# Performance work log

Measured on AMD Instinct MI355X. Metric: run time of the kernel, lower is better.

Reference implementation:

```python
import jax, jax.numpy as jnp
import numpy as np

# Model config (matches init_kwargs)
DATA_L = 256
LATENT_L = 64
LATENT_N = 8
N_COMPS = 8
LOG_2PI = float(np.log(2.0 * np.pi))


def setup_inputs() -> dict:
    key = jax.random.key(0)
    ks = jax.random.split(key, 7)
    B = 2048
    N = B * LATENT_N  # 16384
    x = jax.random.normal(ks[0], (B, DATA_L), dtype=jnp.float32)
    W_e = jax.random.normal(ks[1], (DATA_L, LATENT_L * N_COMPS * 3), dtype=jnp.float32) * 0.05
    b_e = jnp.zeros((LATENT_L * N_COMPS * 3,), dtype=jnp.float32)
    W_d = jax.random.normal(ks[2], (LATENT_L, DATA_L * N_COMPS * 3), dtype=jnp.float32) * 0.05
    b_d = jnp.zeros((DATA_L * N_COMPS * 3,), dtype=jnp.float32)
    u_e = jax.random.normal(ks[3], (N, LATENT_L), dtype=jnp.float32)
    r = jax.random.uniform(ks[4], (N, LATENT_L), dtype=jnp.float32)
    return {"x": x, "W_e": W_e, "b_e": b_e, "W_d": W_d, "b_d": b_d, "u_e": u_e, "r": r}


def _split3(pred, K, D):
    # pred: (N, 3*K*D) -> m, logp, loga each (N, K, D)
    m = pred[:, : K * D].reshape(-1, K, D)
    logp = pred[:, K * D : 2 * K * D].reshape(-1, K, D)
    loga = pred[:, 2 * K * D :].reshape(-1, K, D)
    loga = jax.nn.log_softmax(loga, axis=1)  # loga - logsumexp over comps
    return m, logp, loga


def _discrete_sample(loga, r):
    # loga: (N, K, D), r: (N, D). Matches torch: idx = sum((r > cumsum(p)).int(), dim=1)
    c = jnp.cumsum(jnp.exp(loga), axis=1)  # (N, K, D)
    idx = jnp.sum((r[:, None, :] > c).astype(jnp.int32), axis=1)  # (N, D)
    return jnp.clip(idx, 0, loga.shape[1] - 1)


def reference(x, W_e, b_e, W_d, b_d, u_e, r):
    K, L, D = N_COMPS, LATENT_L, DATA_L
    x_rep = jnp.tile(x, (LATENT_N, 1))  # (N, D)

    # Encoder (KAN with width=[data_l, 3*K*L] modeled as dense layer)
    pred_e = x_rep @ W_e + b_e  # (N, 3*K*L)
    m_e, logp_e, loga_e = _split3(pred_e, K, L)

    # Sample mixture component per (row, latent dim), gather, reparameterize
    idx = _discrete_sample(loga_e, r)  # (N, L) int32
    m_sel = jnp.take_along_axis(m_e, idx[:, None, :], axis=1)[:, 0, :]  # (N, L)
    logp_sel = jnp.take_along_axis(logp_e, idx[:, None, :], axis=1)[:, 0, :]
    h = m_sel + jnp.exp(-0.5 * logp_sel) * u_e  # (N, L)

    # log q(h|x): mixture-of-Gaussians density at h
    uh = jnp.exp(0.5 * logp_e) * (h[:, None, :] - m_e)  # (N, K, L)
    L_e = jax.nn.logsumexp(loga_e - 0.5 * uh * uh + 0.5 * logp_e, axis=1)  # (N, L)
    L_e = -0.5 * L * LOG_2PI + jnp.sum(L_e, axis=1)  # (N,)

    # log prior N(0, I)
    L_q = -0.5 * L * LOG_2PI - 0.5 * jnp.sum(h * h, axis=1)  # (N,)

    # Decoder mixture likelihood of x
    pred_d = h @ W_d + b_d  # (N, 3*K*D)
    m_d, logp_d, loga_d = _split3(pred_d, K, D)
    ux = jnp.exp(0.5 * logp_d) * (x_rep[:, None, :] - m_d)  # (N, K, D)
    L_d = jax.nn.logsumexp(loga_d - 0.5 * ux * ux + 0.5 * logp_d, axis=1)  # (N, D)
    L_d = -0.5 * D * LOG_2PI + jnp.sum(L_d, axis=1)  # (N,)

    return -jnp.mean(L_d + L_q - L_e)
```

## Files before the change

### kernel.cpp

```cpp
#include <hip/hip_runtime.h>
#include <hip/hip_bf16.h>
#include <math.h>

#define D_L   256
#define L_L   64
#define K_C   8
#define BATCH 2048
#define NTOT  16384
#define ENC_COLS 1536
#define DEC_COLS 6144
#define LOG2PI 1.8378770664093453f

typedef __attribute__((ext_vector_type(8)))  short  short8;
typedef __attribute__((ext_vector_type(8)))  unsigned short ushort8;
typedef __attribute__((ext_vector_type(4)))  float  float4_;
typedef __attribute__((ext_vector_type(16))) float  float16_;

#define OFF_PE   0
#define OFF_H    (BATCH * ENC_COLS)
#define OFF_LQE  (OFF_H + NTOT * L_L / 2)
#define OFF_LD   (OFF_LQE + NTOT)
#define OFF_XB   (OFF_LD + NTOT)
#define OFF_WET  (OFF_XB + BATCH * D_L / 2)
#define OFF_WDT  OFF_XB

__device__ __forceinline__ unsigned short f2bf(float f) {
  unsigned u = __float_as_uint(f);
  unsigned r = (u + 0x7fffu + ((u >> 16) & 1u)) >> 16;
  return (unsigned short)r;
}

__global__ __launch_bounds__(256) void k_cvt_x(
    const float* __restrict__ in, unsigned short* __restrict__ out)
{
  const size_t idx = ((size_t)blockIdx.x * 256 + threadIdx.x) * 8;
  float4_ a = *(const float4_*)(in + idx);
  float4_ b = *(const float4_*)(in + idx + 4);
  ushort8 o;
  o[0] = f2bf(a[0]); o[1] = f2bf(a[1]); o[2] = f2bf(a[2]); o[3] = f2bf(a[3]);
  o[4] = f2bf(b[0]); o[5] = f2bf(b[1]); o[6] = f2bf(b[2]); o[7] = f2bf(b[3]);
  *(ushort8*)(out + idx) = o;
}

__global__ __launch_bounds__(256) void k_cvt_T(
    const float* __restrict__ in, unsigned short* __restrict__ out,
    int R, int C)
{
  __shared__ float tile[64][65];
  const int t = threadIdx.x;
  const int c0 = blockIdx.x * 64, r0 = blockIdx.y * 64;
  {
    const int tr = t >> 2, tc = (t & 3) * 16;
    const float* src = in + (size_t)(r0 + tr) * C + c0 + tc;
    #pragma unroll
    for (int i = 0; i < 4; ++i) {
      float4_ v = *(const float4_*)(src + 4 * i);
      #pragma unroll
      for (int j = 0; j < 4; ++j) tile[tr][tc + 4 * i + j] = v[j];
    }
  }
  __syncthreads();
  const int c = t >> 2, ks = (t & 3) * 16;
  unsigned short tmp[16];
  #pragma unroll
  for (int j = 0; j < 16; ++j) tmp[j] = f2bf(tile[ks + j][c]);
  unsigned short* dst = out + (size_t)(c0 + c) * R + r0 + ks;
  ushort8 o0, o1;
  #pragma unroll
  for (int j = 0; j < 8; ++j) { o0[j] = tmp[j]; o1[j] = tmp[8 + j]; }
  *(ushort8*)dst = o0;
  *(ushort8*)(dst + 8) = o1;
}

__global__ __launch_bounds__(256) void k_enc_mfma(
    const unsigned short* __restrict__ xb, const unsigned short* __restrict__ WeT,
    const float* __restrict__ be, float* __restrict__ pe)
{
  __shared__ __align__(16) unsigned short as[64 * 264];
  __shared__ __align__(16) unsigned short bs[64 * 264];
  const int t = threadIdx.x;
  const int w = t >> 6, l = t & 63;
  const int m0 = blockIdx.y * 64, c0 = blockIdx.x * 64;

  #pragma unroll
  for (int p = 0; p < 8; ++p) {
    const int ci = t + 256 * p;
    const int row = ci >> 5, off = (ci & 31) * 8;
    *(ushort8*)&as[row * 264 + off] = *(const ushort8*)(xb + (size_t)(m0 + row) * 256 + off);
    *(ushort8*)&bs[row * 264 + off] = *(const ushort8*)(WeT + (size_t)(c0 + row) * 256 + off);
  }
  __syncthreads();

  const int lr = l & 15, lq = l >> 4;
  float4_ acc[4] = {};
  const unsigned short* aponce = &as[(w * 16 + lr) * 264 + lq * 8];
  #pragma unroll
  for (int kk = 0; kk < 8; ++kk) {
    short8 a = *(const short8*)(aponce + kk * 32);
    #pragma unroll
    for (int ct = 0; ct < 4; ++ct) {
      short8 b = *(const short8*)(&bs[(ct * 16 + lr) * 264 + lq * 8 + kk * 32]);
      acc[ct] = __builtin_amdgcn_mfma_f32_16x16x32_bf16(a, b, acc[ct], 0, 0, 0);
    }
  }
  #pragma unroll
  for (int ct = 0; ct < 4; ++ct) {
    const int c = c0 + ct * 16 + lr;
    const float bias = be[c];
    #pragma unroll
    for (int reg = 0; reg < 4; ++reg) {
      const int m = m0 + w * 16 + lq * 4 + reg;
      pe[(size_t)m * ENC_COLS + c] = acc[ct][reg] + bias;
    }
  }
}

__global__ __launch_bounds__(256) void k_enc_post(
    const float* __restrict__ pe, const float* __restrict__ ue,
    const float* __restrict__ rr, unsigned short* __restrict__ h,
    float* __restrict__ lqe)
{
  const int lane = threadIdx.x & 63;
  const int b = blockIdx.x * 4 + (threadIdx.x >> 6);
  const float* row = pe + (size_t)b * ENC_COLS + lane;

  float m[8], p[8], a[8];
  #pragma unroll
  for (int k = 0; k < K_C; ++k) {
    m[k] = row[k * 64]; p[k] = row[512 + k * 64]; a[k] = row[1024 + k * 64];
  }
  float amax = a[0];
  #pragma unroll
  for (int k = 1; k < K_C; ++k) amax = fmaxf(amax, a[k]);
  float sa = 0.f;
  #pragma unroll
  for (int k = 0; k < K_C; ++k) sa += __expf(a[k] - amax);
  const float lse_a = amax + __logf(sa);

  float cum[8];
  {
    float cs = 0.f;
    #pragma unroll
    for (int k = 0; k < K_C; ++k) { cs += __expf(a[k] - lse_a); cum[k] = cs; }
  }
  float ep[8];
  #pragma unroll
  for (int k = 0; k < K_C; ++k) ep[k] = __expf(p[k]);

  for (int j = 0; j < 8; ++j) {
    const int n = b + BATCH * j;
    const float rv = rr[(size_t)n * L_L + lane];
    const float uv = ue[(size_t)n * L_L + lane];
    int idx = 0;
    #pragma unroll
    for (int k = 0; k < K_C; ++k) idx += (rv > cum[k]) ? 1 : 0;
    idx = min(idx, K_C - 1);
    float msel = m[0], psel = p[0];
    #pragma unroll
    for (int k = 1; k < K_C; ++k) {
      const bool sel = (idx == k);
      msel = sel ? m[k] : msel;
      psel = sel ? p[k] : psel;
    }
    const float hv = fmaf(__expf(-0.5f * psel), uv, msel);
    h[(size_t)n * L_L + lane] = f2bf(hv);

    float st = 0.f;
    #pragma unroll
    for (int k = 0; k < K_C; ++k) {
      const float dd = hv - m[k];
      const float tt = a[k] + 0.5f * p[k] - 0.5f * ep[k] * dd * dd;
      st += __expf(tt);
    }
    float contrib = -0.5f * hv * hv - (__logf(st + 1e-30f) - lse_a);
    #pragma unroll
    for (int off = 32; off; off >>= 1) contrib += __shfl_xor(contrib, off, 64);
    if (lane == 0) lqe[n] = contrib;
  }
}

__global__ void k_zero(float* __restrict__ Ld)
{
  Ld[blockIdx.x * 256 + threadIdx.x] = 0.f;
}

__global__ __launch_bounds__(256) void k_dec_mfma(
    const unsigned short* __restrict__ hb, const float* __restrict__ x,
    const unsigned short* __restrict__ WdT, const float* __restrict__ bd,
    float* __restrict__ Ld)
{
  __shared__ __align__(16) unsigned short hs[64 * 72];
  __shared__ __align__(16) unsigned short bT[192 * 72];
  __shared__ float biasLds[192];

  const int t = threadIdx.x;
  const int w = t >> 6, l = t & 63;
  const int n0 = blockIdx.y * 64, d0 = blockIdx.x * 64;
  const int col = l & 31;
  const int q = l >> 5;
  const int rg = w >> 1;
  const int dg = w & 1;

  #pragma unroll
  for (int p = 0; p < 2; ++p) {
    const int ci = t + 256 * p;
    const int row = ci >> 3, off = (ci & 7) * 8;
    *(ushort8*)&hs[row * 72 + off] = *(const ushort8*)(hb + (size_t)(n0 + row) * 64 + off);
  }

  float xv[16];
  #pragma unroll
  for (int e = 0; e < 16; ++e) {
    const int rr_ = (e & 3) + 8 * (e >> 2) + 4 * q;
    const int n = n0 + rg * 32 + rr_;
    xv[e] = x[(size_t)(n & (BATCH - 1)) * D_L + d0 + dg * 32 + col];
  }

  float s_a[16], s_t[16];
  #pragma unroll
  for (int e = 0; e < 16; ++e) { s_a[e] = 0.f; s_t[e] = 0.f; }

  const unsigned short* arow = &hs[(rg * 32 + col) * 72 + q * 8];
  const unsigned short* brow = &bT[(dg * 32 + col) * 72 + q * 8];

  for (int kc = 0; kc < K_C; ++kc) {
    __syncthreads();
    #pragma unroll
    for (int p = 0; p < 6; ++p) {
      const int ci = t + 256 * p;
      const int c = ci >> 3, off = (ci & 7) * 8;
      const int param = c >> 6, dd = c & 63;
      *(ushort8*)&bT[c * 72 + off] =
          *(const ushort8*)(WdT + ((size_t)param * 2048 + kc * 256 + d0 + dd) * 64 + off);
    }
    if (t < 192) biasLds[t] = bd[(t >> 6) * 2048 + kc * 256 + d0 + (t & 63)];
    __syncthreads();

    float16_ am = {}, ap = {}, aa = {};
    #pragma unroll
    for (int st = 0; st < 4; ++st) {
      short8 af  = *(const short8*)(arow + st * 16);
      short8 bfm = *(const short8*)(brow + st * 16);
      short8 bfp = *(const short8*)(brow + 64 * 72 + st * 16);
      short8 bfa = *(const short8*)(brow + 128 * 72 + st * 16);
      am = __builtin_amdgcn_mfma_f32_32x32x16_bf16(af, bfm, am, 0, 0, 0);
      ap = __builtin_amdgcn_mfma_f32_32x32x16_bf16(af, bfp, ap, 0, 0, 0);
      aa = __builtin_amdgcn_mfma_f32_32x32x16_bf16(af, bfa, aa, 0, 0, 0);
    }

    const float bm_ = biasLds[dg * 32 + col];
    const float bp_ = biasLds[64 + dg * 32 + col];
    const float ba_ = biasLds[128 + dg * 32 + col];
    #pragma unroll
    for (int e = 0; e < 16; ++e) {
      const float lm = am[e] + bm_;
      const float lp = ap[e] + bp_;
      const float la = aa[e] + ba_;
      const float dd = xv[e] - lm;
      const float ex = __expf(lp);
      const float tt = fmaf(0.5f, lp, la) - 0.5f * ex * dd * dd;
      s_a[e] += __expf(la);
      s_t[e] += __expf(tt);
    }
  }

  #pragma unroll
  for (int e = 0; e < 16; ++e) {
    float v = __logf(s_t[e] + 1e-30f) - __logf(s_a[e]);
    v += __shfl_xor(v, 1, 64);
    v += __shfl_xor(v, 2, 64);
    v += __shfl_xor(v, 4, 64);
    v += __shfl_xor(v, 8, 64);
    v += __shfl_xor(v, 16, 64);
    if (col == 0) {
      const int rr_ = (e & 3) + 8 * (e >> 2) + 4 * q;
      atomicAdd(&Ld[n0 + rg * 32 + rr_], v);
    }
  }
}

__global__ __launch_bounds__(1024) void k_final(
    const float* __restrict__ Ld, const float* __restrict__ lqe,
    float* __restrict__ out)
{
  const int tid = threadIdx.x;
  float s = 0.f;
  for (int n = tid; n < NTOT; n += 1024) s += Ld[n] + lqe[n];
  #pragma unroll
  for (int off = 32; off; off >>= 1) s += __shfl_xor(s, off, 64);
  __shared__ float red[16];
  if ((tid & 63) == 0) red[tid >> 6] = s;
  __syncthreads();
  if (tid < 64) {
    float v = (tid < 16) ? red[tid] : 0.f;
    #pragma unroll
    for (int off = 8; off; off >>= 1) v += __shfl_xor(v, off, 64);
    if (tid == 0) out[0] = -(v / (float)NTOT) + 128.0f * LOG2PI;
  }
}

extern "C" void kernel_launch(void* const* d_in, const int* in_sizes, int n_in,
                              void* d_out, int out_size, void* d_ws, size_t ws_size,
                              hipStream_t stream)
{
  const float* x  = (const float*)d_in[0];
  const float* We = (const float*)d_in[1];
  const float* be = (const float*)d_in[2];
  const float* Wd = (const float*)d_in[3];
  const float* bd = (const float*)d_in[4];
  const float* ue = (const float*)d_in[5];
  const float* rr = (const float*)d_in[6];
  float* out = (float*)d_out;

  float* ws = (float*)d_ws;
  float* pe            = ws + OFF_PE;
  unsigned short* h    = (unsigned short*)(ws + OFF_H);
  float* lqe           = ws + OFF_LQE;
  float* Ld            = ws + OFF_LD;
  unsigned short* xb   = (unsigned short*)(ws + OFF_XB);
  unsigned short* WeT  = (unsigned short*)(ws + OFF_WET);
  unsigned short* WdT  = (unsigned short*)(ws + OFF_WDT);

  k_cvt_x<<<dim3(256), 256, 0, stream>>>(x, xb);
  k_cvt_T<<<dim3(ENC_COLS / 64, D_L / 64), 256, 0, stream>>>(We, WeT, D_L, ENC_COLS);
  k_zero<<<dim3(NTOT / 256), 256, 0, stream>>>(Ld);
  k_enc_mfma<<<dim3(ENC_COLS / 64, BATCH / 64), 256, 0, stream>>>(xb, WeT, be, pe);
  k_cvt_T<<<dim3(DEC_COLS / 64, 1), 256, 0, stream>>>(Wd, WdT, L_L, DEC_COLS);
  k_enc_post<<<dim3(BATCH / 4), 256, 0, stream>>>(pe, ue, rr, h, lqe);
  k_dec_mfma<<<dim3(4, NTOT / 64), 256, 0, stream>>>(h, x, WdT, bd, Ld);
  k_final<<<dim3(1), 1024, 0, stream>>>(Ld, lqe, out);
}
```

Before: 140.3 us.

## Restructure pipeline: merged prep kernel, async LDS loads, double-buffered decoder, scalar reduction

Replaces the eight-launch pipeline with five kernels. Weight conversions and accumulator zeroing move into one prep kernel, and the x-to-bf16 conversion is fused into the encoder GEMM, which now uses 32x32 MFMA with K-chunked staging. The decoder now handles 128 rows per block, loads tiles with global_load_lds into double-buffered XOR-swizzled LDS, folds bias and a log2e scale into weights for exp2/log2 math, and reduces straight to one scalar with atomics. This removes launches, intermediate arrays and per-row atomics, at the cost of higher register and LDS use and a non-deterministic float atomic sum.

```diff
diff --git a/kernel.cpp b/kernel.cpp
--- a/kernel.cpp
+++ b/kernel.cpp
@@ -8,120 +8,160 @@
 #define BATCH 2048
 #define NTOT  16384
 #define ENC_COLS 1536
-#define DEC_COLS 6144
 #define LOG2PI 1.8378770664093453f
-
-typedef __attribute__((ext_vector_type(8)))  short  short8;
+#define L2E    1.4426950408889634f
+#define LN2    0.6931471805599453f
+#define C_HL2E 0.7213475204444817f
+
+typedef __attribute__((ext_vector_type(8)))  short short8;
 typedef __attribute__((ext_vector_type(8)))  unsigned short ushort8;
-typedef __attribute__((ext_vector_type(4)))  float  float4_;
-typedef __attribute__((ext_vector_type(16))) float  float16_;
+typedef __attribute__((ext_vector_type(4)))  float float4_;
+typedef __attribute__((ext_vector_type(16))) float float16_;
+
+#if defined(__has_builtin)
+#  if __has_builtin(__builtin_amdgcn_exp2f)
+#    define EXP2F(x) __builtin_amdgcn_exp2f(x)
+#  endif
+#  if __has_builtin(__builtin_amdgcn_logf)
+#    define LOG2F(x) __builtin_amdgcn_logf(x)
+#  endif
+#endif
+#ifndef EXP2F
+#  define EXP2F(x) __expf((x) * LN2)
+#endif
+#ifndef LOG2F
+#  define LOG2F(x) (__logf(x) * L2E)
+#endif
 
 #define OFF_PE   0
 #define OFF_H    (BATCH * ENC_COLS)
-#define OFF_LQE  (OFF_H + NTOT * L_L / 2)
-#define OFF_LD   (OFF_LQE + NTOT)
-#define OFF_XB   (OFF_LD + NTOT)
-#define OFF_WET  (OFF_XB + BATCH * D_L / 2)
-#define OFF_WDT  OFF_XB
+#define OFF_WET  (OFF_H + NTOT * L_L / 2)
+#define OFF_WDT  (OFF_WET + ENC_COLS * D_L / 2)
+#define OFF_ACC  (OFF_WDT + 6144 * 64 / 2)
 
 __device__ __forceinline__ unsigned short f2bf(float f) {
   unsigned u = __float_as_uint(f);
-  unsigned r = (u + 0x7fffu + ((u >> 16) & 1u)) >> 16;
-  return (unsigned short)r;
-}
-
-__global__ __launch_bounds__(256) void k_cvt_x(
-    const float* __restrict__ in, unsigned short* __restrict__ out)
-{
-  const size_t idx = ((size_t)blockIdx.x * 256 + threadIdx.x) * 8;
-  float4_ a = *(const float4_*)(in + idx);
-  float4_ b = *(const float4_*)(in + idx + 4);
-  ushort8 o;
-  o[0] = f2bf(a[0]); o[1] = f2bf(a[1]); o[2] = f2bf(a[2]); o[3] = f2bf(a[3]);
-  o[4] = f2bf(b[0]); o[5] = f2bf(b[1]); o[6] = f2bf(b[2]); o[7] = f2bf(b[3]);
-  *(ushort8*)(out + idx) = o;
-}
-
-__global__ __launch_bounds__(256) void k_cvt_T(
-    const float* __restrict__ in, unsigned short* __restrict__ out,
-    int R, int C)
-{
-  __shared__ float tile[64][65];
-  const int t = threadIdx.x;
-  const int c0 = blockIdx.x * 64, r0 = blockIdx.y * 64;
-  {
-    const int tr = t >> 2, tc = (t & 3) * 16;
-    const float* src = in + (size_t)(r0 + tr) * C + c0 + tc;
-    #pragma unroll
-    for (int i = 0; i < 4; ++i) {
-      float4_ v = *(const float4_*)(src + 4 * i);
-      #pragma unroll
-      for (int j = 0; j < 4; ++j) tile[tr][tc + 4 * i + j] = v[j];
-    }
-  }
-  __syncthreads();
-  const int c = t >> 2, ks = (t & 3) * 16;
-  unsigned short tmp[16];
-  #pragma unroll
-  for (int j = 0; j < 16; ++j) tmp[j] = f2bf(tile[ks + j][c]);
-  unsigned short* dst = out + (size_t)(c0 + c) * R + r0 + ks;
-  ushort8 o0, o1;
-  #pragma unroll
-  for (int j = 0; j < 8; ++j) { o0[j] = tmp[j]; o1[j] = tmp[8 + j]; }
-  *(ushort8*)dst = o0;
-  *(ushort8*)(dst + 8) = o1;
-}
-
-__global__ __launch_bounds__(256) void k_enc_mfma(
-    const unsigned short* __restrict__ xb, const unsigned short* __restrict__ WeT,
+  return (unsigned short)((u + 0x7fffu + ((u >> 16) & 1u)) >> 16);
+}
+
+__device__ __forceinline__ void gll16(const void* g, void* l) {
+  __builtin_amdgcn_global_load_lds(
+      (const __attribute__((address_space(1))) unsigned int*)g,
+      (__attribute__((address_space(3))) unsigned int*)l, 16, 0, 0);
+}
+
+__global__ __launch_bounds__(256) void k_prep(
+    const float* __restrict__ We, const float* __restrict__ Wd,
+    unsigned short* __restrict__ WeT, unsigned short* __restrict__ WdT,
+    float* __restrict__ accf)
+{
+  const int bid = blockIdx.x, t = threadIdx.x;
+  if (bid < 96) {
+    __shared__ float tile[64][65];
+    const int cb = bid % 24, rb = bid / 24;
+    const int c0 = cb * 64, r0 = rb * 64;
+    {
+      const int tr = t >> 2, tc = (t & 3) * 16;
+      const float* src = We + (size_t)(r0 + tr) * ENC_COLS + c0 + tc;
+      #pragma unroll
+      for (int i = 0; i < 4; ++i) {
+        float4_ v = *(const float4_*)(src + 4 * i);
+        #pragma unroll
+        for (int j = 0; j < 4; ++j) tile[tr][tc + 4 * i + j] = v[j];
+      }
+    }
+    __syncthreads();
+    const int c = t >> 2, ks = (t & 3) * 16;
+    ushort8 o0, o1;
+    #pragma unroll
+    for (int j = 0; j < 8; ++j) {
+      o0[j] = f2bf(tile[ks + j][c]);
+      o1[j] = f2bf(tile[ks + 8 + j][c]);
+    }
+    unsigned short* dst = WeT + (size_t)(c0 + c) * D_L + r0 + ks;
+    *(ushort8*)dst = o0;
+    *(ushort8*)(dst + 8) = o1;
+  } else if (bid < 192) {
+    const int idx = bid - 96;
+    const int comp = idx / 12, p = (idx % 12) >> 2, dt = idx & 3;
+    const int c = t & 63, kg = t >> 6;
+    const float scale = (p == 0) ? 1.0f : L2E;
+    const float* src = Wd + (size_t)(kg * 16) * 6144 + p * 2048 + comp * 256 + dt * 64 + c;
+    float v[16];
+    #pragma unroll
+    for (int i = 0; i < 16; ++i) v[i] = src[(size_t)i * 6144] * scale;
+    unsigned short* base = WdT + ((((size_t)(comp * 3 + p) * 4 + dt) * 64 + c) << 6);
+    #pragma unroll
+    for (int j = 0; j < 2; ++j) {
+      ushort8 o;
+      #pragma unroll
+      for (int e = 0; e < 8; ++e) o[e] = f2bf(v[j * 8 + e]);
+      const int ch = (kg * 2 + j) ^ (c & 7);
+      *(ushort8*)(base + ch * 8) = o;
+    }
+  } else {
+    if (t == 0) accf[0] = 0.0f;
+  }
+}
+
+__global__ __launch_bounds__(256) void k_enc(
+    const float* __restrict__ x, const unsigned short* __restrict__ WeT,
     const float* __restrict__ be, float* __restrict__ pe)
 {
-  __shared__ __align__(16) unsigned short as[64 * 264];
-  __shared__ __align__(16) unsigned short bs[64 * 264];
+  __shared__ __align__(16) unsigned short as_[64 * 72];
+  __shared__ __align__(16) unsigned short bs_[64 * 72];
   const int t = threadIdx.x;
   const int w = t >> 6, l = t & 63;
+  const int col = l & 31, q = l >> 5;
+  const int rg = w >> 1, dg = w & 1;
   const int m0 = blockIdx.y * 64, c0 = blockIdx.x * 64;
 
-  #pragma unroll
-  for (int p = 0; p < 8; ++p) {
-    const int ci = t + 256 * p;
-    const int row = ci >> 5, off = (ci & 31) * 8;
-    *(ushort8*)&as[row * 264 + off] = *(const ushort8*)(xb + (size_t)(m0 + row) * 256 + off);
-    *(ushort8*)&bs[row * 264 + off] = *(const ushort8*)(WeT + (size_t)(c0 + row) * 256 + off);
-  }
-  __syncthreads();
-
-  const int lr = l & 15, lq = l >> 4;
-  float4_ acc[4] = {};
-  const unsigned short* aponce = &as[(w * 16 + lr) * 264 + lq * 8];
-  #pragma unroll
-  for (int kk = 0; kk < 8; ++kk) {
-    short8 a = *(const short8*)(aponce + kk * 32);
-    #pragma unroll
-    for (int ct = 0; ct < 4; ++ct) {
-      short8 b = *(const short8*)(&bs[(ct * 16 + lr) * 264 + lq * 8 + kk * 32]);
-      acc[ct] = __builtin_amdgcn_mfma_f32_16x16x32_bf16(a, b, acc[ct], 0, 0, 0);
-    }
-  }
-  #pragma unroll
-  for (int ct = 0; ct < 4; ++ct) {
-    const int c = c0 + ct * 16 + lr;
-    const float bias = be[c];
-    #pragma unroll
-    for (int reg = 0; reg < 4; ++reg) {
-      const int m = m0 + w * 16 + lq * 4 + reg;
-      pe[(size_t)m * ENC_COLS + c] = acc[ct][reg] + bias;
-    }
+  const float bias = be[c0 + dg * 32 + col];
+  float16_ acc;
+  #pragma unroll
+  for (int e = 0; e < 16; ++e) acc[e] = bias;
+
+  for (int kc = 0; kc < 4; ++kc) {
+    if (kc) __syncthreads();
+    #pragma unroll
+    for (int p2 = 0; p2 < 2; ++p2) {
+      const int ci = t + 256 * p2;
+      const int row = ci >> 3, ch = ci & 7;
+      const float* xs = x + (size_t)(m0 + row) * D_L + kc * 64 + ch * 8;
+      float4_ v0 = *(const float4_*)xs;
+      float4_ v1 = *(const float4_*)(xs + 4);
+      ushort8 o;
+      o[0] = f2bf(v0[0]); o[1] = f2bf(v0[1]); o[2] = f2bf(v0[2]); o[3] = f2bf(v0[3]);
+      o[4] = f2bf(v1[0]); o[5] = f2bf(v1[1]); o[6] = f2bf(v1[2]); o[7] = f2bf(v1[3]);
+      *(ushort8*)&as_[row * 72 + ch * 8] = o;
+      *(ushort8*)&bs_[row * 72 + ch * 8] =
+          *(const ushort8*)(WeT + (size_t)(c0 + row) * D_L + kc * 64 + ch * 8);
+    }
+    __syncthreads();
+    const unsigned short* arow = &as_[(rg * 32 + col) * 72 + q * 8];
+    const unsigned short* brow = &bs_[(dg * 32 + col) * 72 + q * 8];
+    #pragma unroll
+    for (int st = 0; st < 4; ++st) {
+      short8 a = *(const short8*)(arow + st * 16);
+      short8 b = *(const short8*)(brow + st * 16);
+      acc = __builtin_amdgcn_mfma_f32_32x32x16_bf16(a, b, acc, 0, 0, 0);
+    }
+  }
+  #pragma unroll
+  for (int e = 0; e < 16; ++e) {
+    const int row = (e & 3) + 8 * (e >> 2) + 4 * q;
+    pe[(size_t)(m0 + rg * 32 + row) * ENC_COLS + c0 + dg * 32 + col] = acc[e];
   }
 }
 
 __global__ __launch_bounds__(256) void k_enc_post(
     const float* __restrict__ pe, const float* __restrict__ ue,
     const float* __restrict__ rr, unsigned short* __restrict__ h,
-    float* __restrict__ lqe)
+    float* __restrict__ accf)
 {
   const int lane = threadIdx.x & 63;
-  const int b = blockIdx.x * 4 + (threadIdx.x >> 6);
+  const int w = threadIdx.x >> 6;
+  const int b = blockIdx.x * 4 + w;
   const float* row = pe + (size_t)b * ENC_COLS + lane;
 
   float m[8], p[8], a[8];
@@ -147,6 +187,9 @@
   #pragma unroll
   for (int k = 0; k < K_C; ++k) ep[k] = __expf(p[k]);
 
+  const int sw = ((((lane >> 3) ^ (b & 7)) << 3) | (lane & 7));
+
+  float tot = 0.f;
   for (int j = 0; j < 8; ++j) {
     const int n = b + BATCH * j;
     const float rv = rr[(size_t)n * L_L + lane];
@@ -163,7 +206,7 @@
       psel = sel ? p[k] : psel;
     }
     const float hv = fmaf(__expf(-0.5f * psel), uv, msel);
-    h[(size_t)n * L_L + lane] = f2bf(hv);
+    h[(size_t)n * L_L + sw] = f2bf(hv);
 
     float st = 0.f;
     #pragma unroll
@@ -172,131 +215,151 @@
       const float tt = a[k] + 0.5f * p[k] - 0.5f * ep[k] * dd * dd;
       st += __expf(tt);
     }
-    float contrib = -0.5f * hv * hv - (__logf(st + 1e-30f) - lse_a);
-    #pragma unroll
-    for (int off = 32; off; off >>= 1) contrib += __shfl_xor(contrib, off, 64);
-    if (lane == 0) lqe[n] = contrib;
-  }
-}
-
-__global__ void k_zero(float* __restrict__ Ld)
-{
-  Ld[blockIdx.x * 256 + threadIdx.x] = 0.f;
-}
-
-__global__ __launch_bounds__(256) void k_dec_mfma(
+    tot += -0.5f * hv * hv - (__logf(st + 1e-30f) - lse_a);
+  }
+  #pragma unroll
+  for (int off = 1; off < 64; off <<= 1) tot += __shfl_xor(tot, off, 64);
+  __shared__ float red2[4];
+  if (lane == 0) red2[w] = tot;
+  __syncthreads();
+  if (threadIdx.x == 0) atomicAdd(accf, red2[0] + red2[1] + red2[2] + red2[3]);
+}
+
+__global__ __launch_bounds__(256, 2) void k_dec(
     const unsigned short* __restrict__ hb, const float* __restrict__ x,
     const unsigned short* __restrict__ WdT, const float* __restrict__ bd,
-    float* __restrict__ Ld)
-{
-  __shared__ __align__(16) unsigned short hs[64 * 72];
-  __shared__ __align__(16) unsigned short bT[192 * 72];
-  __shared__ float biasLds[192];
+    float* __restrict__ accf)
+{
+  __shared__ __align__(16) unsigned short hs[128 * 64];
+  __shared__ __align__(16) unsigned short bT[2][3 * 64 * 64];
+  __shared__ float biasLds[1536];
 
   const int t = threadIdx.x;
   const int w = t >> 6, l = t & 63;
-  const int n0 = blockIdx.y * 64, d0 = blockIdx.x * 64;
-  const int col = l & 31;
-  const int q = l >> 5;
-  const int rg = w >> 1;
-  const int dg = w & 1;
-
-  #pragma unroll
-  for (int p = 0; p < 2; ++p) {
-    const int ci = t + 256 * p;
-    const int row = ci >> 3, off = (ci & 7) * 8;
-    *(ushort8*)&hs[row * 72 + off] = *(const ushort8*)(hb + (size_t)(n0 + row) * 64 + off);
-  }
-
-  float xv[16];
-  #pragma unroll
-  for (int e = 0; e < 16; ++e) {
-    const int rr_ = (e & 3) + 8 * (e >> 2) + 4 * q;
-    const int n = n0 + rg * 32 + rr_;
-    xv[e] = x[(size_t)(n & (BATCH - 1)) * D_L + d0 + dg * 32 + col];
-  }
-
-  float s_a[16], s_t[16];
-  #pragma unroll
-  for (int e = 0; e < 16; ++e) { s_a[e] = 0.f; s_t[e] = 0.f; }
-
-  const unsigned short* arow = &hs[(rg * 32 + col) * 72 + q * 8];
-  const unsigned short* brow = &bT[(dg * 32 + col) * 72 + q * 8];
+  const int col = l & 31, q = l >> 5, c7 = col & 7;
+  const int rg = w >> 1, dg = w & 1;
+  const int dt = blockIdx.x, d0 = dt * 64;
+  const int n0 = blockIdx.y * 128;
+
+  {
+    const char* hg = (const char*)hb + (size_t)n0 * 128;
+    #pragma unroll
+    for (int j = 0; j < 4; ++j) {
+      const int cj = (w << 2) | j;
+      gll16(hg + cj * 1024 + l * 16, (char*)hs + cj * 1024);
+    }
+  }
+  #pragma unroll
+  for (int p = 0; p < 3; ++p) {
+    const char* gsrc = (const char*)WdT + (((size_t)p * 4 + dt) << 13);
+    #pragma unroll
+    for (int j = 0; j < 2; ++j) {
+      const int cj = (w << 1) | j;
+      gll16(gsrc + cj * 1024 + l * 16, (char*)bT[0] + p * 8192 + cj * 1024);
+    }
+  }
+  #pragma unroll
+  for (int i = 0; i < 6; ++i) {
+    const int idx = t + 256 * i;
+    const int pp = idx >> 9, comp = (idx >> 6) & 7, d = idx & 63;
+    float v = bd[pp * 2048 + comp * 256 + d0 + d];
+    if (pp) v *= L2E;
+    biasLds[idx] = v;
+  }
+  float xv[2][16];
+  #pragma unroll
+  for (int t2 = 0; t2 < 2; ++t2)
+    #pragma unroll
+    for (int e = 0; e < 16; ++e) {
+      const int rw = (e & 3) + 8 * (e >> 2) + 4 * q;
+      const int n = n0 + t2 * 64 + rg * 32 + rw;
+      xv[t2][e] = x[(size_t)(n & (BATCH - 1)) * D_L + d0 + dg * 32 + col];
+    }
+
+  __syncthreads();
+
+  short8 af[2][4];
+  #pragma unroll
+  for (int t2 = 0; t2 < 2; ++t2)
+    #pragma unroll
+    for (int st = 0; st < 4; ++st) {
+      const int ch = ((st * 2 + q) ^ c7);
+      af[t2][st] = *(const short8*)((const char*)hs + t2 * 8192 +
+                                    (rg * 32 + col) * 128 + ch * 16);
+    }
+
+  float s_a[2][16], s_t[2][16];
+  #pragma unroll
+  for (int t2 = 0; t2 < 2; ++t2)
+    #pragma unroll
+    for (int e = 0; e < 16; ++e) { s_a[t2][e] = 0.f; s_t[t2][e] = 0.f; }
+
+  const int browoff = (dg * 32 + col) * 128;
 
   for (int kc = 0; kc < K_C; ++kc) {
+    if (kc < 7) {
+      #pragma unroll
+      for (int p = 0; p < 3; ++p) {
+        const char* gsrc = (const char*)WdT + (((size_t)((kc + 1) * 3 + p) * 4 + dt) << 13);
+        #pragma unroll
+        for (int j = 0; j < 2; ++j) {
+          const int cj = (w << 1) | j;
+          gll16(gsrc + cj * 1024 + l * 16,
+                (char*)bT[(kc + 1) & 1] + p * 8192 + cj * 1024);
+        }
+      }
+    }
+    const float bm = biasLds[kc * 64 + dg * 32 + col];
+    const float bp = biasLds[512 + kc * 64 + dg * 32 + col];
+    const float ba = biasLds[1024 + kc * 64 + dg * 32 + col];
+    const char* bbuf = (const char*)bT[kc & 1];
+
+    #pragma unroll
+    for (int t2 = 0; t2 < 2; ++t2) {
+      float16_ am, ap, aa;
+      #pragma unroll
+      for (int e = 0; e < 16; ++e) { am[e] = bm; ap[e] = bp; aa[e] = ba; }
+      #pragma unroll
+      for (int st = 0; st < 4; ++st) {
+        const int ch = ((st * 2 + q) ^ c7) * 16;
+        short8 wm_ = *(const short8*)(bbuf + browoff + ch);
+        short8 wp_ = *(const short8*)(bbuf + 8192 + browoff + ch);
+        short8 wa_ = *(const short8*)(bbuf + 16384 + browoff + ch);
+        am = __builtin_amdgcn_mfma_f32_32x32x16_bf16(af[t2][st], wm_, am, 0, 0, 0);
+        ap = __builtin_amdgcn_mfma_f32_32x32x16_bf16(af[t2][st], wp_, ap, 0, 0, 0);
+        aa = __builtin_amdgcn_mfma_f32_32x32x16_bf16(af[t2][st], wa_, aa, 0, 0, 0);
+      }
+      #pragma unroll
+      for (int e = 0; e < 16; ++e) {
+        const float dd = xv[t2][e] - am[e];
+        const float ex2 = EXP2F(ap[e]);
+        const float t1 = fmaf(0.5f, ap[e], aa[e]);
+        const float ttL = fmaf(-C_HL2E * ex2, dd * dd, t1);
+        s_a[t2][e] += EXP2F(aa[e]);
+        s_t[t2][e] += EXP2F(ttL);
+      }
+    }
     __syncthreads();
-    #pragma unroll
-    for (int p = 0; p < 6; ++p) {
-      const int ci = t + 256 * p;
-      const int c = ci >> 3, off = (ci & 7) * 8;
-      const int param = c >> 6, dd = c & 63;
-      *(ushort8*)&bT[c * 72 + off] =
-          *(const ushort8*)(WdT + ((size_t)param * 2048 + kc * 256 + d0 + dd) * 64 + off);
-    }
-    if (t < 192) biasLds[t] = bd[(t >> 6) * 2048 + kc * 256 + d0 + (t & 63)];
-    __syncthreads();
-
-    float16_ am = {}, ap = {}, aa = {};
-    #pragma unroll
-    for (int st = 0; st < 4; ++st) {
-      short8 af  = *(const short8*)(arow + st * 16);
-      short8 bfm = *(const short8*)(brow + st * 16);
-      short8 bfp = *(const short8*)(brow + 64 * 72 + st * 16);
-      short8 bfa = *(const short8*)(brow + 128 * 72 + st * 16);
-      am = __builtin_amdgcn_mfma_f32_32x32x16_bf16(af, bfm, am, 0, 0, 0);
-      ap = __builtin_amdgcn_mfma_f32_32x32x16_bf16(af, bfp, ap, 0, 0, 0);
-      aa = __builtin_amdgcn_mfma_f32_32x32x16_bf16(af, bfa, aa, 0, 0, 0);
-    }
-
-    const float bm_ = biasLds[dg * 32 + col];
-    const float bp_ = biasLds[64 + dg * 32 + col];
-    const float ba_ = biasLds[128 + dg * 32 + col];
-    #pragma unroll
-    for (int e = 0; e < 16; ++e) {
-      const float lm = am[e] + bm_;
-      const float lp = ap[e] + bp_;
-      const float la = aa[e] + ba_;
-      const float dd = xv[e] - lm;
-      const float ex = __expf(lp);
-      const float tt = fmaf(0.5f, lp, la) - 0.5f * ex * dd * dd;
-      s_a[e] += __expf(la);
-      s_t[e] += __expf(tt);
-    }
-  }
-
-  #pragma unroll
-  for (int e = 0; e < 16; ++e) {
-    float v = __logf(s_t[e] + 1e-30f) - __logf(s_a[e]);
-    v += __shfl_xor(v, 1, 64);
-    v += __shfl_xor(v, 2, 64);
-    v += __shfl_xor(v, 4, 64);
-    v += __shfl_xor(v, 8, 64);
-    v += __shfl_xor(v, 16, 64);
-    if (col == 0) {
-      const int rr_ = (e & 3) + 8 * (e >> 2) + 4 * q;
-      atomicAdd(&Ld[n0 + rg * 32 + rr_], v);
-    }
-  }
-}
-
-__global__ __launch_bounds__(1024) void k_final(
-    const float* __restrict__ Ld, const float* __restrict__ lqe,
-    float* __restrict__ out)
-{
-  const int tid = threadIdx.x;
-  float s = 0.f;
-  for (int n = tid; n < NTOT; n += 1024) s += Ld[n] + lqe[n];
-  #pragma unroll
-  for (int off = 32; off; off >>= 1) s += __shfl_xor(s, off, 64);
-  __shared__ float red[16];
-  if ((tid & 63) == 0) red[tid >> 6] = s;
+  }
+
+  float v = 0.f;
+  #pragma unroll
+  for (int t2 = 0; t2 < 2; ++t2)
+    #pragma unroll
+    for (int e = 0; e < 16; ++e)
+      v += LOG2F(s_t[t2][e] + 1e-30f) - LOG2F(s_a[t2][e]);
+  v *= LN2;
+  #pragma unroll
+  for (int off = 1; off < 64; off <<= 1) v += __shfl_xor(v, off, 64);
+  float* red = (float*)hs;
+  if (l == 0) red[w] = v;
   __syncthreads();
-  if (tid < 64) {
-    float v = (tid < 16) ? red[tid] : 0.f;
-    #pragma unroll
-    for (int off = 8; off; off >>= 1) v += __shfl_xor(v, off, 64);
-    if (tid == 0) out[0] = -(v / (float)NTOT) + 128.0f * LOG2PI;
-  }
+  if (t == 0) atomicAdd(accf, red[0] + red[1] + red[2] + red[3]);
+}
+
+__global__ void k_final(const float* __restrict__ accf, float* __restrict__ out)
+{
+  if (threadIdx.x == 0) out[0] = -(accf[0] / (float)NTOT) + 128.0f * LOG2PI;
 }
 
 extern "C" void kernel_launch(void* const* d_in, const int* in_sizes, int n_in,
@@ -313,20 +376,15 @@
   float* out = (float*)d_out;
 
   float* ws = (float*)d_ws;
-  float* pe            = ws + OFF_PE;
-  unsigned short* h    = (unsigned short*)(ws + OFF_H);
-  float* lqe           = ws + OFF_LQE;
-  float* Ld            = ws + OFF_LD;
-  unsigned short* xb   = (unsigned short*)(ws + OFF_XB);
-  unsigned short* WeT  = (unsigned short*)(ws + OFF_WET);
-  unsigned short* WdT  = (unsigned short*)(ws + OFF_WDT);
-
-  k_cvt_x<<<dim3(256), 256, 0, stream>>>(x, xb);
-  k_cvt_T<<<dim3(ENC_COLS / 64, D_L / 64), 256, 0, stream>>>(We, WeT, D_L, ENC_COLS);
-  k_zero<<<dim3(NTOT / 256), 256, 0, stream>>>(Ld);
-  k_enc_mfma<<<dim3(ENC_COLS / 64, BATCH / 64), 256, 0, stream>>>(xb, WeT, be, pe);
-  k_cvt_T<<<dim3(DEC_COLS / 64, 1), 256, 0, stream>>>(Wd, WdT, L_L, DEC_COLS);
-  k_enc_post<<<dim3(BATCH / 4), 256, 0, stream>>>(pe, ue, rr, h, lqe);
-  k_dec_mfma<<<dim3(4, NTOT / 64), 256, 0, stream>>>(h, x, WdT, bd, Ld);
-  k_final<<<dim3(1), 1024, 0, stream>>>(Ld, lqe, out);
-}
+  float* pe           = ws + OFF_PE;
+  unsigned short* h   = (unsigned short*)(ws + OFF_H);
+  unsigned short* WeT = (unsigned short*)(ws + OFF_WET);
+  unsigned short* WdT = (unsigned short*)(ws + OFF_WDT);
+  float* accf         = ws + OFF_ACC;
+
+  k_prep<<<dim3(193), 256, 0, stream>>>(We, Wd, WeT, WdT, accf);
+  k_enc<<<dim3(ENC_COLS / 64, BATCH / 64), 256, 0, stream>>>(x, WeT, be, pe);
+  k_enc_post<<<dim3(BATCH / 4), 256, 0, stream>>>(pe, ue, rr, h, accf);
+  k_dec<<<dim3(4, NTOT / 128), 256, 0, stream>>>(h, x, WdT, bd, accf);
+  k_final<<<dim3(1), 64, 0, stream>>>(accf, out);
+}
```

New measurement: 134.1 us. -4.4%, faster.
